# Kernel optimization log

Hardware: AMD Instinct MI355X
Metric: run time of the kernel (lower is better)

## Reference

```python
import jax, jax.numpy as jnp
import numpy as np

B, S, DIM, BITS, HEXPERTS = 4, 4096, 2048, 32, 4


def setup_inputs() -> dict:
    key = jax.random.key(0)
    ks = jax.random.split(key, 6)
    scale = 1.0 / np.sqrt(DIM)
    return {
        "x": jax.random.normal(ks[0], (B, S, DIM), dtype=jnp.float32),
        "A1_w": jax.random.normal(ks[1], (BITS, DIM), dtype=jnp.float32) * scale,
        "A1_b": jax.random.normal(ks[2], (BITS,), dtype=jnp.float32) * 0.01,
        "emb": jax.random.normal(ks[3], (BITS, DIM), dtype=jnp.float32),
        "aggr_w": jax.random.normal(ks[4], (HEXPERTS,), dtype=jnp.float32) * 0.5,
        "aggr_b": jax.random.normal(ks[5], (1,), dtype=jnp.float32) * 0.01,
    }


def reference(x, A1_w, A1_b, emb, aggr_w, aggr_b):
    # Router: small linear [B,S,DIM] -> [B,S,BITS], softmax over bits.
    logits = jnp.einsum("bsd,kd->bsk", x, A1_w) + A1_b
    h_c = jax.nn.softmax(logits, axis=-1)
    # Top-k expert selection (k = Hexperts = 4), sorted descending like torch.topk.
    v, i = jax.lax.top_k(h_c, HEXPERTS)  # v,i: [B,S,4]
    # Gather expert embeddings: [B,S,4,DIM]
    h_emb = emb[i]
    # Scale by gate values and combine across experts with the 4->1 linear.
    # expert_aggr(h_emb.transpose(-2,-1)) == sum_e v[...,e]*h_emb[...,e,:]*w[e] + b
    out = jnp.einsum("bse,bsed,e->bsd", v, h_emb, aggr_w) + aggr_b[0]
    # Residual multiply (dropout p=0 -> identity).
    return x * out
```

## Files before the change

kernel.cpp:

```cpp
#include <hip/hip_runtime.h>


#define NTOK 16384
#define DIMV 2048

typedef const __attribute__((address_space(1))) unsigned int* as1_u32p;
typedef __attribute__((address_space(3))) unsigned int* as3_u32p;

__global__ __launch_bounds__(512, 4) void router_k(
    const float* __restrict__ x,
    const float* __restrict__ A1w,
    const float* __restrict__ A1b,
    const float* __restrict__ aggw,
    float* __restrict__ gates)
{
    __shared__ float smem[9216];

    const int tid  = threadIdx.x;
    const int lane = tid & 63;
    const int wid  = tid >> 6;
    const int t    = lane & 31;
    const int h    = lane >> 5;
    const int tok0 = blockIdx.x << 5;
    const int dbase = wid << 8;

    float* wstage = smem + (wid << 10);

    const float* xrow = x + (size_t)(tok0 + t) * DIMV + dbase + (h << 3);

    const float* wsrc_base = A1w + (size_t)(lane >> 2) * DIMV + dbase
                           + ((lane & 3) << 2);

    float acc[32];
    #pragma unroll
    for (int k = 0; k < 32; ++k) acc[k] = 0.f;

    #pragma unroll
    for (int j = 0; j < 2; ++j)
        __builtin_amdgcn_global_load_lds(
            (as1_u32p)(const void*)(wsrc_base + (size_t)(j << 4) * DIMV),
            (as3_u32p)(void*)(wstage + (j << 8)), 16, 0, 0);
    float4 xa = *(const float4*)(xrow);
    float4 xb = *(const float4*)(xrow + 4);
    asm volatile("s_waitcnt vmcnt(0)" ::: "memory");

    int buf = 0;
    for (int c = 0; c < 16; ++c) {
        float4 xna, xnb;
        if (c < 15) {
            const float* src = wsrc_base + ((c + 1) << 4);
            float* dst = wstage + ((buf ^ 1) << 9);
            #pragma unroll
            for (int j = 0; j < 2; ++j)
                __builtin_amdgcn_global_load_lds(
                    (as1_u32p)(const void*)(src + (size_t)(j << 4) * DIMV),
                    (as3_u32p)(void*)(dst + (j << 8)), 16, 0, 0);
            xna = *(const float4*)(xrow + ((c + 1) << 4));
            xnb = *(const float4*)(xrow + ((c + 1) << 4) + 4);
        }
        const float* wb = wstage + (buf << 9);
        #pragma unroll
        for (int k = 0; k < 32; ++k) {
            const float4 w0 = *(const float4*)&wb[(k << 4) + (h << 3)];
            const float4 w1 = *(const float4*)&wb[(k << 4) + (h << 3) + 4];
            float a = acc[k];
            a = fmaf(xa.x, w0.x, a); a = fmaf(xa.y, w0.y, a);
            a = fmaf(xa.z, w0.z, a); a = fmaf(xa.w, w0.w, a);
            a = fmaf(xb.x, w1.x, a); a = fmaf(xb.y, w1.y, a);
            a = fmaf(xb.z, w1.z, a); a = fmaf(xb.w, w1.w, a);
            acc[k] = a;
        }
        asm volatile("s_waitcnt vmcnt(0)" ::: "memory");
        xa = xna; xb = xnb; buf ^= 1;
    }

    #pragma unroll
    for (int k = 0; k < 32; ++k) acc[k] += __shfl_xor(acc[k], 32);

    __syncthreads();
    float* red = smem;
    if (lane < 32) {
        float* r = red + wid * 1152 + t * 36;
        #pragma unroll
        for (int q = 0; q < 8; ++q)
            *(float4*)&r[q << 2] = make_float4(acc[4*q], acc[4*q+1],
                                               acc[4*q+2], acc[4*q+3]);
    }
    __syncthreads();

    if (tid < 32) {
        const int tt = tid;
        float l[32];
        #pragma unroll
        for (int q = 0; q < 8; ++q) {
            float4 v = make_float4(0.f, 0.f, 0.f, 0.f);
            #pragma unroll
            for (int w = 0; w < 8; ++w) {
                const float4 p = *(const float4*)&red[w * 1152 + tt * 36 + (q << 2)];
                v.x += p.x; v.y += p.y; v.z += p.z; v.w += p.w;
            }
            l[4*q]   = v.x + A1b[4*q];
            l[4*q+1] = v.y + A1b[4*q+1];
            l[4*q+2] = v.z + A1b[4*q+2];
            l[4*q+3] = v.w + A1b[4*q+3];
        }
        float m = l[0];
        #pragma unroll
        for (int k = 1; k < 32; ++k) m = fmaxf(m, l[k]);
        float s = 0.f;
        #pragma unroll
        for (int k = 0; k < 32; ++k) { l[k] = expf(l[k] - m); s += l[k]; }
        const float inv = 1.0f / s;

        unsigned used = 0u;
        float gv[4]; unsigned iv[4];
        #pragma unroll
        for (int e = 0; e < 4; ++e) {
            float best = -1.f; int bi = 0;
            #pragma unroll
            for (int k = 0; k < 32; ++k) {
                bool ok = !((used >> k) & 1u) && (l[k] > best);
                best = ok ? l[k] : best;
                bi   = ok ? k    : bi;
            }
            used |= (1u << bi);
            gv[e] = best * inv * aggw[e];
            iv[e] = (unsigned)bi;
        }
        float* gp = gates + (size_t)(tok0 + tt) * 8;
        *(float4*)gp = make_float4(gv[0], gv[1], gv[2], gv[3]);
        *(float4*)(gp + 4) = make_float4(__uint_as_float(iv[0]), __uint_as_float(iv[1]),
                                         __uint_as_float(iv[2]), __uint_as_float(iv[3]));
    }
}

__global__ __launch_bounds__(256) void moe_out_k(
    const float* __restrict__ x,
    const float* __restrict__ emb,
    const float* __restrict__ gates,
    const float* __restrict__ aggb,
    float* __restrict__ out)
{
    const int t   = blockIdx.x;
    const int tid = threadIdx.x;
    const float* gp = gates + (size_t)t * 8;
    const float4 g  = *(const float4*)gp;
    const float4 ibits = *(const float4*)(gp + 4);
    const unsigned i0 = __float_as_uint(ibits.x);
    const unsigned i1 = __float_as_uint(ibits.y);
    const unsigned i2 = __float_as_uint(ibits.z);
    const unsigned i3 = __float_as_uint(ibits.w);
    const float b = aggb[0];
    const size_t base = (size_t)t * DIMV;

    #pragma unroll
    for (int h = 0; h < DIMV; h += 1024) {
        const int d = h + (tid << 2);
        const float4 xv = *(const float4*)&x[base + d];
        const float4 e0 = *(const float4*)&emb[(size_t)i0 * DIMV + d];
        const float4 e1 = *(const float4*)&emb[(size_t)i1 * DIMV + d];
        const float4 e2 = *(const float4*)&emb[(size_t)i2 * DIMV + d];
        const float4 e3 = *(const float4*)&emb[(size_t)i3 * DIMV + d];
        float4 a, o;
        a.x = fmaf(g.x, e0.x, fmaf(g.y, e1.x, fmaf(g.z, e2.x, fmaf(g.w, e3.x, b))));
        a.y = fmaf(g.x, e0.y, fmaf(g.y, e1.y, fmaf(g.z, e2.y, fmaf(g.w, e3.y, b))));
        a.z = fmaf(g.x, e0.z, fmaf(g.y, e1.z, fmaf(g.z, e2.z, fmaf(g.w, e3.z, b))));
        a.w = fmaf(g.x, e0.w, fmaf(g.y, e1.w, fmaf(g.z, e2.w, fmaf(g.w, e3.w, b))));
        o.x = xv.x * a.x; o.y = xv.y * a.y; o.z = xv.z * a.z; o.w = xv.w * a.w;
        *(float4*)&out[base + d] = o;
    }
}

extern "C" void kernel_launch(void* const* d_in, const int* in_sizes, int n_in,
                              void* d_out, int out_size, void* d_ws, size_t ws_size,
                              hipStream_t stream)
{
    (void)in_sizes; (void)n_in; (void)out_size; (void)ws_size;
    const float* x    = (const float*)d_in[0];
    const float* A1w  = (const float*)d_in[1];
    const float* A1b  = (const float*)d_in[2];
    const float* emb  = (const float*)d_in[3];
    const float* aggw = (const float*)d_in[4];
    const float* aggb = (const float*)d_in[5];
    float* out   = (float*)d_out;
    float* gates = (float*)d_ws;

    router_k<<<NTOK / 32, 512, 0, stream>>>(x, A1w, A1b, aggw, gates);
    moe_out_k<<<NTOK, 256, 0, stream>>>(x, emb, gates, aggb, out);
}
```

Before: 104.0 us.

## Load router weights directly from global and compute two tokens per lane

```diff
diff --git a/kernel.cpp b/kernel.cpp
--- a/kernel.cpp
+++ b/kernel.cpp
@@ -3,9 +3,6 @@
 
 #define NTOK 16384
 #define DIMV 2048
-
-typedef const __attribute__((address_space(1))) unsigned int* as1_u32p;
-typedef __attribute__((address_space(3))) unsigned int* as3_u32p;
 
 __global__ __launch_bounds__(512, 4) void router_k(
     const float* __restrict__ x,
@@ -19,72 +16,59 @@
     const int tid  = threadIdx.x;
     const int lane = tid & 63;
     const int wid  = tid >> 6;
-    const int t    = lane & 31;
-    const int h    = lane >> 5;
+    const int t    = lane & 15;
+    const int h    = lane >> 4;
     const int tok0 = blockIdx.x << 5;
-    const int dbase = wid << 8;
+    const int dbase = (wid << 8) + (h << 2);
 
-    float* wstage = smem + (wid << 10);
+    const float* xrowA = x + (size_t)(tok0 + t)      * DIMV + dbase;
+    const float* xrowB = x + (size_t)(tok0 + t + 16) * DIMV + dbase;
+    const float* wbase = A1w + dbase;
 
-    const float* xrow = x + (size_t)(tok0 + t) * DIMV + dbase + (h << 3);
+    float acc0[32], acc1[32];
+    #pragma unroll
+    for (int k = 0; k < 32; ++k) { acc0[k] = 0.f; acc1[k] = 0.f; }
 
-    const float* wsrc_base = A1w + (size_t)(lane >> 2) * DIMV + dbase
-                           + ((lane & 3) << 2);
+    float4 xa = *(const float4*)(xrowA);
+    float4 xb = *(const float4*)(xrowB);
 
-    float acc[32];
-    #pragma unroll
-    for (int k = 0; k < 32; ++k) acc[k] = 0.f;
-
-    #pragma unroll
-    for (int j = 0; j < 2; ++j)
-        __builtin_amdgcn_global_load_lds(
-            (as1_u32p)(const void*)(wsrc_base + (size_t)(j << 4) * DIMV),
-            (as3_u32p)(void*)(wstage + (j << 8)), 16, 0, 0);
-    float4 xa = *(const float4*)(xrow);
-    float4 xb = *(const float4*)(xrow + 4);
-    asm volatile("s_waitcnt vmcnt(0)" ::: "memory");
-
-    int buf = 0;
     for (int c = 0; c < 16; ++c) {
-        float4 xna, xnb;
-        if (c < 15) {
-            const float* src = wsrc_base + ((c + 1) << 4);
-            float* dst = wstage + ((buf ^ 1) << 9);
-            #pragma unroll
-            for (int j = 0; j < 2; ++j)
-                __builtin_amdgcn_global_load_lds(
-                    (as1_u32p)(const void*)(src + (size_t)(j << 4) * DIMV),
-                    (as3_u32p)(void*)(dst + (j << 8)), 16, 0, 0);
-            xna = *(const float4*)(xrow + ((c + 1) << 4));
-            xnb = *(const float4*)(xrow + ((c + 1) << 4) + 4);
-        }
-        const float* wb = wstage + (buf << 9);
+        const int cn = (c < 15) ? (c + 1) : 15;
+        const float4 xna = *(const float4*)(xrowA + (cn << 4));
+        const float4 xnb = *(const float4*)(xrowB + (cn << 4));
+        const float* wc = wbase + (c << 4);
         #pragma unroll
         for (int k = 0; k < 32; ++k) {
-            const float4 w0 = *(const float4*)&wb[(k << 4) + (h << 3)];
-            const float4 w1 = *(const float4*)&wb[(k << 4) + (h << 3) + 4];
-            float a = acc[k];
-            a = fmaf(xa.x, w0.x, a); a = fmaf(xa.y, w0.y, a);
-            a = fmaf(xa.z, w0.z, a); a = fmaf(xa.w, w0.w, a);
-            a = fmaf(xb.x, w1.x, a); a = fmaf(xb.y, w1.y, a);
-            a = fmaf(xb.z, w1.z, a); a = fmaf(xb.w, w1.w, a);
-            acc[k] = a;
+            const float4 w = *(const float4*)(wc + k * DIMV);
+            float a = acc0[k], b = acc1[k];
+            a = fmaf(xa.x, w.x, a); a = fmaf(xa.y, w.y, a);
+            a = fmaf(xa.z, w.z, a); a = fmaf(xa.w, w.w, a);
+            b = fmaf(xb.x, w.x, b); b = fmaf(xb.y, w.y, b);
+            b = fmaf(xb.z, w.z, b); b = fmaf(xb.w, w.w, b);
+            acc0[k] = a; acc1[k] = b;
         }
-        asm volatile("s_waitcnt vmcnt(0)" ::: "memory");
-        xa = xna; xb = xnb; buf ^= 1;
+        xa = xna; xb = xnb;
     }
 
     #pragma unroll
-    for (int k = 0; k < 32; ++k) acc[k] += __shfl_xor(acc[k], 32);
+    for (int k = 0; k < 32; ++k) {
+        float a = acc0[k], b = acc1[k];
+        a += __shfl_xor(a, 16); a += __shfl_xor(a, 32);
+        b += __shfl_xor(b, 16); b += __shfl_xor(b, 32);
+        acc0[k] = a; acc1[k] = b;
+    }
 
-    __syncthreads();
     float* red = smem;
-    if (lane < 32) {
-        float* r = red + wid * 1152 + t * 36;
+    if (lane < 16) {
+        float* r0 = red + wid * 1152 + t * 36;
+        float* r1 = red + wid * 1152 + (t + 16) * 36;
         #pragma unroll
-        for (int q = 0; q < 8; ++q)
-            *(float4*)&r[q << 2] = make_float4(acc[4*q], acc[4*q+1],
-                                               acc[4*q+2], acc[4*q+3]);
+        for (int q = 0; q < 8; ++q) {
+            *(float4*)&r0[q << 2] = make_float4(acc0[4*q], acc0[4*q+1],
+                                                acc0[4*q+2], acc0[4*q+3]);
+            *(float4*)&r1[q << 2] = make_float4(acc1[4*q], acc1[4*q+1],
+                                                acc1[4*q+2], acc1[4*q+3]);
+        }
     }
     __syncthreads();
 
```

Measured after the change: 153.8 us. +47.9%, slower.

## Read router weights directly from global memory instead of LDS staging

Applied to the files above, without the earlier changes.

```diff
diff --git a/kernel.cpp b/kernel.cpp
--- a/kernel.cpp
+++ b/kernel.cpp
@@ -3,9 +3,6 @@
 
 #define NTOK 16384
 #define DIMV 2048
-
-typedef const __attribute__((address_space(1))) unsigned int* as1_u32p;
-typedef __attribute__((address_space(3))) unsigned int* as3_u32p;
 
 __global__ __launch_bounds__(512, 4) void router_k(
     const float* __restrict__ x,
@@ -22,62 +19,35 @@
     const int t    = lane & 31;
     const int h    = lane >> 5;
     const int tok0 = blockIdx.x << 5;
-    const int dbase = wid << 8;
+    const int dbase = (wid << 8) + (h << 2);
 
-    float* wstage = smem + (wid << 10);
-
-    const float* xrow = x + (size_t)(tok0 + t) * DIMV + dbase + (h << 3);
-
-    const float* wsrc_base = A1w + (size_t)(lane >> 2) * DIMV + dbase
-                           + ((lane & 3) << 2);
+    const float* xrow  = x   + (size_t)(tok0 + t) * DIMV + dbase;
+    const float* wbase = A1w + dbase;
 
     float acc[32];
     #pragma unroll
     for (int k = 0; k < 32; ++k) acc[k] = 0.f;
 
-    #pragma unroll
-    for (int j = 0; j < 2; ++j)
-        __builtin_amdgcn_global_load_lds(
-            (as1_u32p)(const void*)(wsrc_base + (size_t)(j << 4) * DIMV),
-            (as3_u32p)(void*)(wstage + (j << 8)), 16, 0, 0);
-    float4 xa = *(const float4*)(xrow);
-    float4 xb = *(const float4*)(xrow + 4);
-    asm volatile("s_waitcnt vmcnt(0)" ::: "memory");
+    float4 xv = *(const float4*)(xrow);
 
-    int buf = 0;
-    for (int c = 0; c < 16; ++c) {
-        float4 xna, xnb;
-        if (c < 15) {
-            const float* src = wsrc_base + ((c + 1) << 4);
-            float* dst = wstage + ((buf ^ 1) << 9);
-            #pragma unroll
-            for (int j = 0; j < 2; ++j)
-                __builtin_amdgcn_global_load_lds(
-                    (as1_u32p)(const void*)(src + (size_t)(j << 4) * DIMV),
-                    (as3_u32p)(void*)(dst + (j << 8)), 16, 0, 0);
-            xna = *(const float4*)(xrow + ((c + 1) << 4));
-            xnb = *(const float4*)(xrow + ((c + 1) << 4) + 4);
-        }
-        const float* wb = wstage + (buf << 9);
+    for (int c = 0; c < 32; ++c) {
+        const int cn = (c < 31) ? (c + 1) : 31;
+        const float4 xn = *(const float4*)(xrow + (cn << 3));
+        const float* wc = wbase + (c << 3);
         #pragma unroll
         for (int k = 0; k < 32; ++k) {
-            const float4 w0 = *(const float4*)&wb[(k << 4) + (h << 3)];
-            const float4 w1 = *(const float4*)&wb[(k << 4) + (h << 3) + 4];
+            const float4 w = *(const float4*)(wc + k * DIMV);
             float a = acc[k];
-            a = fmaf(xa.x, w0.x, a); a = fmaf(xa.y, w0.y, a);
-            a = fmaf(xa.z, w0.z, a); a = fmaf(xa.w, w0.w, a);
-            a = fmaf(xb.x, w1.x, a); a = fmaf(xb.y, w1.y, a);
-            a = fmaf(xb.z, w1.z, a); a = fmaf(xb.w, w1.w, a);
+            a = fmaf(xv.x, w.x, a); a = fmaf(xv.y, w.y, a);
+            a = fmaf(xv.z, w.z, a); a = fmaf(xv.w, w.w, a);
             acc[k] = a;
         }
-        asm volatile("s_waitcnt vmcnt(0)" ::: "memory");
-        xa = xna; xb = xnb; buf ^= 1;
+        xv = xn;
     }
 
     #pragma unroll
     for (int k = 0; k < 32; ++k) acc[k] += __shfl_xor(acc[k], 32);
 
-    __syncthreads();
     float* red = smem;
     if (lane < 32) {
         float* r = red + wid * 1152 + t * 36;
```

New measurement: 221.3 us. 2.13x slower.
